# Kernel optimization log

Hardware: AMD Instinct MI355X
Metric: run time of the kernel (lower is better)

## Reference

```python
import jax, jax.numpy as jnp
import numpy as np

ALPHA_LO = float(np.exp(-1.0 / 5.0))   # 0.8187
ALPHA_HI = float(np.exp(-1.0 / 25.0))  # 0.9608
BN_EPS = 1e-5

B, T, D_IN, H = 32, 2000, 512, 512


def setup_inputs() -> dict:
    key = jax.random.key(0)
    ks = jax.random.split(key, 5)
    x = jax.random.normal(ks[0], (B, T, D_IN), dtype=jnp.float32)
    W = jax.random.normal(ks[1], (H, D_IN), dtype=jnp.float32) / np.sqrt(D_IN)
    b = jax.random.normal(ks[2], (H,), dtype=jnp.float32) * 0.01
    alpha = jax.random.uniform(ks[3], (H,), dtype=jnp.float32,
                               minval=ALPHA_LO, maxval=ALPHA_HI)
    gamma = jnp.ones((H,), dtype=jnp.float32)
    beta = jnp.zeros((H,), dtype=jnp.float32)
    ut0 = jax.random.uniform(ks[4], (B, H), dtype=jnp.float32)
    return {"x": x, "W": W, "b": b, "alpha": alpha,
            "gamma": gamma, "beta": beta, "ut0": ut0}


def reference(x, W, b, alpha, gamma, beta, ut0):
    # Linear: [B,T,Din] @ [Din,H] + b
    Wx = jnp.einsum("btd,hd->bth", x, W) + b
    # BatchNorm1d (training forward): stats over flattened (B*T) dim
    flat = Wx.reshape(-1, Wx.shape[-1])
    mean = flat.mean(axis=0)
    var = flat.var(axis=0)  # biased, as torch BN uses for normalization
    Wx = ((flat - mean) * jax.lax.rsqrt(var + BN_EPS) * gamma + beta).reshape(Wx.shape)
    # Readout cell: leaky integration + softmax accumulation over time
    a = jnp.clip(alpha, ALPHA_LO, ALPHA_HI)

    def step(carry, wxt):
        ut, acc = carry
        ut = a * ut + (1.0 - a) * wxt          # [B,H]
        acc = acc + jax.nn.softmax(ut, axis=1)
        return (ut, acc), None

    wx_t = jnp.transpose(Wx, (1, 0, 2))  # [T,B,H]
    (_, out), _ = jax.lax.scan(step, (ut0, jnp.zeros_like(ut0)), wx_t)
    return out[:, None, :]  # [B,1,H]
```

## Files before the change

kernel.cpp:

```cpp
#include <hip/hip_runtime.h>
#include <hip/hip_bf16.h>
#include <stdint.h>


namespace {
constexpr int kB = 32;
constexpr int kT = 2000;
constexpr int kD = 512;
constexpr int kH = 512;
constexpr int kM = kB * kT;
constexpr int kBM = 128;
constexpr int kNB = kM / kBM;
constexpr int kL = 16;
constexpr int kC = kT / kL;
constexpr int kG = 5;
constexpr int kNG = kC / kG;
constexpr float kALo = 0.81873075307798182f;
constexpr float kAHi = 0.96078943915232320f;

typedef __bf16 bf16x8 __attribute__((ext_vector_type(8)));
typedef float floatx16 __attribute__((ext_vector_type(16)));

__device__ __forceinline__ float bf2f(unsigned short u) {
  return __builtin_bit_cast(float, (unsigned)u << 16);
}
__device__ __forceinline__ float clipa(float a) {
  return fminf(fmaxf(a, kALo), kAHi);
}
__device__ __forceinline__ float pow16(float a) {
  const float a2 = a * a, a4 = a2 * a2, a8 = a4 * a4;
  return a8 * a8;
}
__device__ __forceinline__ void gld_lds16(const void* g, void* l) {
  __builtin_amdgcn_global_load_lds(
      (const __attribute__((address_space(1))) uint32_t*)g,
      (__attribute__((address_space(3))) uint32_t*)(uintptr_t)l, 16, 0, 0);
}

__global__ __launch_bounds__(256) void wcvt_k(const float* __restrict__ W,
                                              __bf16* __restrict__ Wbf) {
  const int t = blockIdx.x * 256 + threadIdx.x;
  const float4 a0 = ((const float4*)W)[t * 2];
  const float4 a1 = ((const float4*)W)[t * 2 + 1];
  bf16x8 v;
  v[0] = (__bf16)a0.x; v[1] = (__bf16)a0.y; v[2] = (__bf16)a0.z; v[3] = (__bf16)a0.w;
  v[4] = (__bf16)a1.x; v[5] = (__bf16)a1.y; v[6] = (__bf16)a1.z; v[7] = (__bf16)a1.w;
  const int h = t >> 6, k8 = t & 63;
  *(bf16x8*)(Wbf + ((size_t)k8 * 512 + h) * 8) = v;
}

__global__ __launch_bounds__(512, 2) void gemm_k(const float* __restrict__ X,
                                                 const __bf16* __restrict__ Wbf,
                                                 const float* __restrict__ alpha,
                                                 unsigned short* __restrict__ Wxb,
                                                 float* __restrict__ vbuf,
                                                 float* __restrict__ partial) {
  __shared__ alignas(16) __bf16 As2[2][4][128][8];
  __shared__ alignas(16) bf16x8 Bs2[2][2048];
  __shared__ float sred[2][kH];
  const int tid = threadIdx.x;
  const size_t row0 = (size_t)blockIdx.x * kBM;
  const int w = tid >> 6, L = tid & 63;
  const int ct0 = w * 2;
  const int lhalf = L >> 5, l32 = L & 31;
  const int arow = tid >> 2, akq = tid & 3;

  floatx16 acc[4][2] = {};
  const float* xptr = X + (row0 + arow) * kD + akq * 8;

  float4 a0 = *(const float4*)xptr;
  float4 a1 = *(const float4*)(xptr + 4);
#pragma unroll
  for (int j = 0; j < 4; ++j) {
    const int ci = j * 512 + tid;
    gld_lds16(Wbf + (size_t)ci * 8, (char*)&Bs2[0][0] + (size_t)ci * 16);
  }
  {
    bf16x8 av;
    av[0] = (__bf16)a0.x; av[1] = (__bf16)a0.y; av[2] = (__bf16)a0.z; av[3] = (__bf16)a0.w;
    av[4] = (__bf16)a1.x; av[5] = (__bf16)a1.y; av[6] = (__bf16)a1.z; av[7] = (__bf16)a1.w;
    *(bf16x8*)&As2[0][akq][arow][0] = av;
  }
  a0 = *(const float4*)(xptr + 32);
  a1 = *(const float4*)(xptr + 36);
  asm volatile("s_waitcnt vmcnt(2) lgkmcnt(0)" ::: "memory");
  __builtin_amdgcn_s_barrier();

#pragma unroll 1
  for (int s = 0; s < 16; ++s) {
    const int buf = s & 1;
    if (s < 15) {
#pragma unroll
      for (int j = 0; j < 4; ++j) {
        const int ci = j * 512 + tid;
        gld_lds16(Wbf + ((size_t)(s + 1) * 2048 + ci) * 8,
                  (char*)&Bs2[buf ^ 1][0] + (size_t)ci * 16);
      }
      bf16x8 av;
      av[0] = (__bf16)a0.x; av[1] = (__bf16)a0.y; av[2] = (__bf16)a0.z; av[3] = (__bf16)a0.w;
      av[4] = (__bf16)a1.x; av[5] = (__bf16)a1.y; av[6] = (__bf16)a1.z; av[7] = (__bf16)a1.w;
      *(bf16x8*)&As2[buf ^ 1][akq][arow][0] = av;
      if (s < 14) {
        a0 = *(const float4*)(xptr + (s + 2) * 32);
        a1 = *(const float4*)(xptr + (s + 2) * 32 + 4);
      }
    }
#pragma unroll
    for (int kh = 0; kh < 2; ++kh) {
      const int kq = kh * 2 + lhalf;
      const bf16x8 af0 = *(const bf16x8*)&As2[buf][kq][l32][0];
      const bf16x8 af1 = *(const bf16x8*)&As2[buf][kq][32 + l32][0];
      const bf16x8 af2 = *(const bf16x8*)&As2[buf][kq][64 + l32][0];
      const bf16x8 af3 = *(const bf16x8*)&As2[buf][kq][96 + l32][0];
      const bf16x8 b0 = Bs2[buf][kq * 512 + ct0 * 32 + l32];
      const bf16x8 b1 = Bs2[buf][kq * 512 + (ct0 + 1) * 32 + l32];
      acc[0][0] = __builtin_amdgcn_mfma_f32_32x32x16_bf16(af0, b0, acc[0][0], 0, 0, 0);
      acc[0][1] = __builtin_amdgcn_mfma_f32_32x32x16_bf16(af0, b1, acc[0][1], 0, 0, 0);
      acc[1][0] = __builtin_amdgcn_mfma_f32_32x32x16_bf16(af1, b0, acc[1][0], 0, 0, 0);
      acc[1][1] = __builtin_amdgcn_mfma_f32_32x32x16_bf16(af1, b1, acc[1][1], 0, 0, 0);
      acc[2][0] = __builtin_amdgcn_mfma_f32_32x32x16_bf16(af2, b0, acc[2][0], 0, 0, 0);
      acc[2][1] = __builtin_amdgcn_mfma_f32_32x32x16_bf16(af2, b1, acc[2][1], 0, 0, 0);
      acc[3][0] = __builtin_amdgcn_mfma_f32_32x32x16_bf16(af3, b0, acc[3][0], 0, 0, 0);
      acc[3][1] = __builtin_amdgcn_mfma_f32_32x32x16_bf16(af3, b1, acc[3][1], 0, 0, 0);
    }
    if (s < 15) {
      if (s < 14)
        asm volatile("s_waitcnt vmcnt(2) lgkmcnt(0)" ::: "memory");
      else
        asm volatile("s_waitcnt vmcnt(0) lgkmcnt(0)" ::: "memory");
      __builtin_amdgcn_s_barrier();
    }
  }

  __syncthreads();
  sred[0][tid] = 0.f;
  sred[1][tid] = 0.f;
  __syncthreads();
#pragma unroll
  for (int c = 0; c < 2; ++c) {
    float s = 0.f, q = 0.f;
#pragma unroll
    for (int rt = 0; rt < 4; ++rt) {
#pragma unroll
      for (int r = 0; r < 16; ++r) {
        const float v = acc[rt][c][r];
        s += v;
        q += v * v;
      }
    }
    s += __shfl_xor(s, 32);
    q += __shfl_xor(q, 32);
    if (lhalf == 0) {
      atomicAdd(&sred[0][(ct0 + c) * 32 + l32], s);
      atomicAdd(&sred[1][(ct0 + c) * 32 + l32], q);
    }
  }

#pragma unroll
  for (int c = 0; c < 2; ++c) {
    const int col = (ct0 + c) * 32 + l32;
    const float a = clipa(alpha[col]);
    const float oma = 1.0f - a;
    const float a2 = a * a, a4 = a2 * a2, a8 = a4 * a4;
    float wgt[8];
    wgt[0] = a8 * a2 * a; wgt[1] = a8 * a2; wgt[2] = a8 * a; wgt[3] = a8;
    wgt[4] = a2 * a;      wgt[5] = a2;      wgt[6] = a;      wgt[7] = 1.0f;
    const float mult = (lhalf == 0) ? a4 * oma : oma;
#pragma unroll
    for (int j = 0; j < 8; ++j) wgt[j] *= mult;
#pragma unroll
    for (int rt = 0; rt < 4; ++rt) {
#pragma unroll
      for (int c32 = 0; c32 < 2; ++c32) {
        float S = 0.f;
#pragma unroll
        for (int j = 0; j < 8; ++j) S += wgt[j] * acc[rt][c][c32 * 8 + j];
        S += __shfl_xor(S, 32);
        if (lhalf == 0) {
          const int g = (int)(row0 >> 4) + rt * 2 + c32;
          vbuf[(size_t)g * kH + col] = S;
        }
      }
    }
  }

#pragma unroll
  for (int rt = 0; rt < 4; ++rt) {
#pragma unroll
    for (int c = 0; c < 2; ++c) {
      const int col = (ct0 + c) * 32 + l32;
#pragma unroll
      for (int r = 0; r < 16; ++r) {
        const int row = rt * 32 + 4 * lhalf + (r & 3) + 8 * (r >> 2);
        const unsigned short u = __builtin_bit_cast(unsigned short, (__bf16)acc[rt][c][r]);
        const unsigned un = __shfl_down((unsigned)u, 1);
        if ((l32 & 1) == 0)
          *(unsigned*)(Wxb + (row0 + row) * (size_t)kH + col) = (unsigned)u | (un << 16);
      }
    }
  }
  __syncthreads();
  partial[(size_t)blockIdx.x * 1024 + tid] = sred[0][tid];
  partial[(size_t)blockIdx.x * 1024 + 512 + tid] = sred[1][tid];
}

__global__ __launch_bounds__(512) void red1_k(const float* __restrict__ partial,
                                              float* __restrict__ sums) {
  const int tid = threadIdx.x;
  const int r0 = blockIdx.x * 20;
  float s0 = 0.f, s1 = 0.f;
#pragma unroll 5
  for (int r = 0; r < 20; ++r) {
    s0 += partial[(size_t)(r0 + r) * 1024 + tid];
    s1 += partial[(size_t)(r0 + r) * 1024 + 512 + tid];
  }
  atomicAdd(&sums[tid], s0);
  atomicAdd(&sums[kH + tid], s1);
}

__global__ __launch_bounds__(512) void fin_scan_k(const float* __restrict__ sums,
                                                  const float* __restrict__ alpha,
                                                  const float* __restrict__ gamma,
                                                  const float* __restrict__ beta,
                                                  const float* __restrict__ ut0,
                                                  float* __restrict__ prm,
                                                  const float* __restrict__ vbuf,
                                                  float* __restrict__ ustart) {
  const int h = threadIdx.x;
  const int b = blockIdx.x;
  const float inv_n = 1.0f / (float)kM;
  const float mean = sums[h] * inv_n;
  const float var = sums[kH + h] * inv_n - mean * mean;
  const float sc = gamma[h] * rsqrtf(var + 1e-5f);
  const float sh = beta[h] - mean * sc;
  const float a = clipa(alpha[h]);
  if (b == 0) {
    prm[h] = sc;
    prm[kH + h] = sh;
    prm[2 * kH + h] = a;
    prm[3 * kH + h] = 1.0f - a;
  }
  const float a16 = pow16(a);
  const float shc = sh * (1.0f - a16);
  float u = ut0[(size_t)b * kH + h];
  float vc[kG];
#pragma unroll 1
  for (int cb = 0; cb < kC; cb += kG) {
#pragma unroll
    for (int j = 0; j < kG; ++j)
      vc[j] = vbuf[((size_t)b * kC + cb + j) * kH + h];
    ustart[((size_t)b * kNG + cb / kG) * kH + h] = u;
#pragma unroll
    for (int j = 0; j < kG; ++j) u = a16 * u + sc * vc[j] + shc;
  }
}

__global__ __launch_bounds__(512) void soft_k(const unsigned short* __restrict__ Wxb,
                                              const float* __restrict__ prm,
                                              const float* __restrict__ ustart,
                                              float* __restrict__ out) {
  __shared__ float part[kL][9];
  __shared__ float zinv[kL];
  const int bc = blockIdx.x;
  const int b = bc / kNG, grp = bc % kNG;
  const int h = threadIdx.x;
  const int wv = h >> 6, lane = h & 63;
  const float sc = prm[h], sh = prm[kH + h];
  const float a = prm[2 * kH + h], oma = prm[3 * kH + h];
  float u = ustart[(size_t)bc * kH + h];
  const unsigned short* base =
      Wxb + ((size_t)b * kT + (size_t)grp * kG * kL) * kH + h;
  float acc = 0.f;
#pragma unroll 1
  for (int cc = 0; cc < kG; ++cc) {
    float e[kL];
#pragma unroll
    for (int i = 0; i < kL; ++i) {
      const float wvx = bf2f(base[(size_t)(cc * kL + i) * kH]) * sc + sh;
      u = a * u + oma * wvx;
      e[i] = __expf(u);
    }
#pragma unroll
    for (int i = 0; i < kL; ++i) {
      float s = e[i];
#pragma unroll
      for (int off = 32; off > 0; off >>= 1) s += __shfl_xor(s, off);
      if (lane == 0) part[i][wv] = s;
    }
    __syncthreads();
    if (h < kL) {
      float s = 0.f;
#pragma unroll
      for (int j = 0; j < 8; ++j) s += part[h][j];
      zinv[h] = 1.0f / s;
    }
    __syncthreads();
#pragma unroll
    for (int i = 0; i < kL; ++i) acc += e[i] * zinv[i];
    __syncthreads();
  }
  atomicAdd(&out[(size_t)b * kH + h], acc);
}

}

extern "C" void kernel_launch(void* const* d_in, const int* in_sizes, int n_in,
                              void* d_out, int out_size, void* d_ws, size_t ws_size,
                              hipStream_t stream) {
  const float* x = (const float*)d_in[0];
  const float* Wm = (const float*)d_in[1];
  const float* alpha = (const float*)d_in[3];
  const float* gamma = (const float*)d_in[4];
  const float* beta = (const float*)d_in[5];
  const float* ut0 = (const float*)d_in[6];
  float* out = (float*)d_out;

  float* wsp = (float*)d_ws;
  float* vbuf = wsp;
  float* ustart = vbuf + (size_t)kB * kC * kH;
  float* partial = ustart + (size_t)kB * kNG * kH;
  float* sums = partial + (size_t)500 * 1024;
  float* prm = sums + 2 * kH;
  __bf16* Wbf = (__bf16*)(prm + 4 * kH);
  unsigned short* Wxb = (unsigned short*)(Wbf + (size_t)kH * kD);

  hipMemsetAsync(sums, 0, 2 * kH * sizeof(float), stream);
  hipMemsetAsync(out, 0, (size_t)kB * kH * sizeof(float), stream);
  wcvt_k<<<128, 256, 0, stream>>>(Wm, Wbf);
  gemm_k<<<kNB, 512, 0, stream>>>(x, Wbf, alpha, Wxb, vbuf, partial);
  red1_k<<<25, 512, 0, stream>>>(partial, sums);
  fin_scan_k<<<kB, 512, 0, stream>>>(sums, alpha, gamma, beta, ut0, prm, vbuf, ustart);
  soft_k<<<kB * kNG, 512, 0, stream>>>(Wxb, prm, ustart, out);
}
```

Measured before the change: 301.4 us.

## Halve GEMM row tile and read W fragments directly from global memory

```diff
diff --git a/kernel.cpp b/kernel.cpp
--- a/kernel.cpp
+++ b/kernel.cpp
@@ -9,7 +9,7 @@
 constexpr int kD = 512;
 constexpr int kH = 512;
 constexpr int kM = kB * kT;
-constexpr int kBM = 128;
+constexpr int kBM = 64;
 constexpr int kNB = kM / kBM;
 constexpr int kL = 16;
 constexpr int kC = kT / kL;
@@ -18,6 +18,7 @@
 constexpr float kALo = 0.81873075307798182f;
 constexpr float kAHi = 0.96078943915232320f;
 
+typedef __bf16 bf16x4 __attribute__((ext_vector_type(4)));
 typedef __bf16 bf16x8 __attribute__((ext_vector_type(8)));
 typedef float floatx16 __attribute__((ext_vector_type(16)));
 
@@ -30,11 +31,6 @@
 __device__ __forceinline__ float pow16(float a) {
   const float a2 = a * a, a4 = a2 * a2, a8 = a4 * a4;
   return a8 * a8;
-}
-__device__ __forceinline__ void gld_lds16(const void* g, void* l) {
-  __builtin_amdgcn_global_load_lds(
-      (const __attribute__((address_space(1))) uint32_t*)g,
-      (__attribute__((address_space(3))) uint32_t*)(uintptr_t)l, 16, 0, 0);
 }
 
 __global__ __launch_bounds__(256) void wcvt_k(const float* __restrict__ W,
@@ -49,85 +45,63 @@
   *(bf16x8*)(Wbf + ((size_t)k8 * 512 + h) * 8) = v;
 }
 
-__global__ __launch_bounds__(512, 2) void gemm_k(const float* __restrict__ X,
+__global__ __launch_bounds__(512, 4) void gemm_k(const float* __restrict__ X,
                                                  const __bf16* __restrict__ Wbf,
                                                  const float* __restrict__ alpha,
                                                  unsigned short* __restrict__ Wxb,
                                                  float* __restrict__ vbuf,
                                                  float* __restrict__ partial) {
-  __shared__ alignas(16) __bf16 As2[2][4][128][8];
-  __shared__ alignas(16) bf16x8 Bs2[2][2048];
+  __shared__ alignas(16) __bf16 As2[2][4][65][8];
   __shared__ float sred[2][kH];
   const int tid = threadIdx.x;
   const size_t row0 = (size_t)blockIdx.x * kBM;
   const int w = tid >> 6, L = tid & 63;
   const int ct0 = w * 2;
   const int lhalf = L >> 5, l32 = L & 31;
-  const int arow = tid >> 2, akq = tid & 3;
-
-  floatx16 acc[4][2] = {};
-  const float* xptr = X + (row0 + arow) * kD + akq * 8;
+  const int arow = tid >> 3, acol = (tid & 7) * 4;
+  const int akq = acol >> 3, aoff = acol & 7;
+
+  floatx16 acc[2][2] = {};
+  const float* xptr = X + (row0 + arow) * kD + acol;
+  const __bf16* bptr = Wbf + ((size_t)(ct0 * 32) + l32) * 8;
 
   float4 a0 = *(const float4*)xptr;
-  float4 a1 = *(const float4*)(xptr + 4);
-#pragma unroll
-  for (int j = 0; j < 4; ++j) {
-    const int ci = j * 512 + tid;
-    gld_lds16(Wbf + (size_t)ci * 8, (char*)&Bs2[0][0] + (size_t)ci * 16);
-  }
   {
-    bf16x8 av;
-    av[0] = (__bf16)a0.x; av[1] = (__bf16)a0.y; av[2] = (__bf16)a0.z; av[3] = (__bf16)a0.w;
-    av[4] = (__bf16)a1.x; av[5] = (__bf16)a1.y; av[6] = (__bf16)a1.z; av[7] = (__bf16)a1.w;
-    *(bf16x8*)&As2[0][akq][arow][0] = av;
+    bf16x4 av;
+    av[0] = (__bf16)a0.x; av[1] = (__bf16)a0.y;
+    av[2] = (__bf16)a0.z; av[3] = (__bf16)a0.w;
+    *(bf16x4*)&As2[0][akq][arow][aoff] = av;
   }
   a0 = *(const float4*)(xptr + 32);
-  a1 = *(const float4*)(xptr + 36);
-  asm volatile("s_waitcnt vmcnt(2) lgkmcnt(0)" ::: "memory");
+  asm volatile("s_waitcnt lgkmcnt(0)" ::: "memory");
   __builtin_amdgcn_s_barrier();
 
 #pragma unroll 1
   for (int s = 0; s < 16; ++s) {
     const int buf = s & 1;
     if (s < 15) {
-#pragma unroll
-      for (int j = 0; j < 4; ++j) {
-        const int ci = j * 512 + tid;
-        gld_lds16(Wbf + ((size_t)(s + 1) * 2048 + ci) * 8,
-                  (char*)&Bs2[buf ^ 1][0] + (size_t)ci * 16);
-      }
-      bf16x8 av;
-      av[0] = (__bf16)a0.x; av[1] = (__bf16)a0.y; av[2] = (__bf16)a0.z; av[3] = (__bf16)a0.w;
-      av[4] = (__bf16)a1.x; av[5] = (__bf16)a1.y; av[6] = (__bf16)a1.z; av[7] = (__bf16)a1.w;
-      *(bf16x8*)&As2[buf ^ 1][akq][arow][0] = av;
-      if (s < 14) {
+      bf16x4 av;
+      av[0] = (__bf16)a0.x; av[1] = (__bf16)a0.y;
+      av[2] = (__bf16)a0.z; av[3] = (__bf16)a0.w;
+      *(bf16x4*)&As2[buf ^ 1][akq][arow][aoff] = av;
+      if (s < 14)
         a0 = *(const float4*)(xptr + (s + 2) * 32);
-        a1 = *(const float4*)(xptr + (s + 2) * 32 + 4);
-      }
     }
 #pragma unroll
     for (int kh = 0; kh < 2; ++kh) {
       const int kq = kh * 2 + lhalf;
+      const __bf16* bq = bptr + (size_t)(s * 4 + kq) * 4096;
+      const bf16x8 b0 = *(const bf16x8*)bq;
+      const bf16x8 b1 = *(const bf16x8*)(bq + 256);
       const bf16x8 af0 = *(const bf16x8*)&As2[buf][kq][l32][0];
       const bf16x8 af1 = *(const bf16x8*)&As2[buf][kq][32 + l32][0];
-      const bf16x8 af2 = *(const bf16x8*)&As2[buf][kq][64 + l32][0];
-      const bf16x8 af3 = *(const bf16x8*)&As2[buf][kq][96 + l32][0];
-      const bf16x8 b0 = Bs2[buf][kq * 512 + ct0 * 32 + l32];
-      const bf16x8 b1 = Bs2[buf][kq * 512 + (ct0 + 1) * 32 + l32];
       acc[0][0] = __builtin_amdgcn_mfma_f32_32x32x16_bf16(af0, b0, acc[0][0], 0, 0, 0);
       acc[0][1] = __builtin_amdgcn_mfma_f32_32x32x16_bf16(af0, b1, acc[0][1], 0, 0, 0);
       acc[1][0] = __builtin_amdgcn_mfma_f32_32x32x16_bf16(af1, b0, acc[1][0], 0, 0, 0);
       acc[1][1] = __builtin_amdgcn_mfma_f32_32x32x16_bf16(af1, b1, acc[1][1], 0, 0, 0);
-      acc[2][0] = __builtin_amdgcn_mfma_f32_32x32x16_bf16(af2, b0, acc[2][0], 0, 0, 0);
-      acc[2][1] = __builtin_amdgcn_mfma_f32_32x32x16_bf16(af2, b1, acc[2][1], 0, 0, 0);
-      acc[3][0] = __builtin_amdgcn_mfma_f32_32x32x16_bf16(af3, b0, acc[3][0], 0, 0, 0);
-      acc[3][1] = __builtin_amdgcn_mfma_f32_32x32x16_bf16(af3, b1, acc[3][1], 0, 0, 0);
     }
     if (s < 15) {
-      if (s < 14)
-        asm volatile("s_waitcnt vmcnt(2) lgkmcnt(0)" ::: "memory");
-      else
-        asm volatile("s_waitcnt vmcnt(0) lgkmcnt(0)" ::: "memory");
+      asm volatile("s_waitcnt lgkmcnt(0)" ::: "memory");
       __builtin_amdgcn_s_barrier();
     }
   }
@@ -140,7 +114,7 @@
   for (int c = 0; c < 2; ++c) {
     float s = 0.f, q = 0.f;
 #pragma unroll
-    for (int rt = 0; rt < 4; ++rt) {
+    for (int rt = 0; rt < 2; ++rt) {
 #pragma unroll
       for (int r = 0; r < 16; ++r) {
         const float v = acc[rt][c][r];
@@ -169,7 +143,7 @@
 #pragma unroll
     for (int j = 0; j < 8; ++j) wgt[j] *= mult;
 #pragma unroll
-    for (int rt = 0; rt < 4; ++rt) {
+    for (int rt = 0; rt < 2; ++rt) {
 #pragma unroll
       for (int c32 = 0; c32 < 2; ++c32) {
         float S = 0.f;
@@ -177,7 +151,7 @@
         for (int j = 0; j < 8; ++j) S += wgt[j] * acc[rt][c][c32 * 8 + j];
         S += __shfl_xor(S, 32);
         if (lhalf == 0) {
-          const int g = (int)(row0 >> 4) + rt * 2 + c32;
+          const int g = (int)blockIdx.x * 4 + rt * 2 + c32;
           vbuf[(size_t)g * kH + col] = S;
         }
       }
@@ -185,7 +159,7 @@
   }
 
 #pragma unroll
-  for (int rt = 0; rt < 4; ++rt) {
+  for (int rt = 0; rt < 2; ++rt) {
 #pragma unroll
     for (int c = 0; c < 2; ++c) {
       const int col = (ct0 + c) * 32 + l32;
@@ -207,10 +181,10 @@
 __global__ __launch_bounds__(512) void red1_k(const float* __restrict__ partial,
                                               float* __restrict__ sums) {
   const int tid = threadIdx.x;
-  const int r0 = blockIdx.x * 20;
+  const int r0 = blockIdx.x * 25;
   float s0 = 0.f, s1 = 0.f;
 #pragma unroll 5
-  for (int r = 0; r < 20; ++r) {
+  for (int r = 0; r < 25; ++r) {
     s0 += partial[(size_t)(r0 + r) * 1024 + tid];
     s1 += partial[(size_t)(r0 + r) * 1024 + 512 + tid];
   }
@@ -319,7 +293,7 @@
   float* vbuf = wsp;
   float* ustart = vbuf + (size_t)kB * kC * kH;
   float* partial = ustart + (size_t)kB * kNG * kH;
-  float* sums = partial + (size_t)500 * 1024;
+  float* sums = partial + (size_t)1000 * 1024;
   float* prm = sums + 2 * kH;
   __bf16* Wbf = (__bf16*)(prm + 4 * kH);
   unsigned short* Wxb = (unsigned short*)(Wbf + (size_t)kH * kD);
@@ -328,7 +302,7 @@
   hipMemsetAsync(out, 0, (size_t)kB * kH * sizeof(float), stream);
   wcvt_k<<<128, 256, 0, stream>>>(Wm, Wbf);
   gemm_k<<<kNB, 512, 0, stream>>>(x, Wbf, alpha, Wxb, vbuf, partial);
-  red1_k<<<25, 512, 0, stream>>>(partial, sums);
+  red1_k<<<40, 512, 0, stream>>>(partial, sums);
   fin_scan_k<<<kB, 512, 0, stream>>>(sums, alpha, gamma, beta, ut0, prm, vbuf, ustart);
   soft_k<<<kB * kNG, 512, 0, stream>>>(Wxb, prm, ustart, out);
 }
```

New measurement: 304.8 us. About the same (+1.2%).
